# Performance work log

Hardware: AMD Instinct MI355X
Metric: run time of the kernel (lower is better)

The kernel has to match this reference:

```python
import jax, jax.numpy as jnp
import numpy as np

NUM_HEADS = 16
D_MODEL = 1024
D_K = D_MODEL // NUM_HEADS
THETA = 10000.0
SEQ_LEN = 2048
BATCH = 2


def _rope(x, token_positions):
    # x: [B, H, S, d_k]; token_positions: [S] int
    d_k = x.shape[-1]
    inv_freq = THETA ** (-jnp.arange(0, d_k, 2, dtype=jnp.float32) / d_k)  # [d_k/2]
    ang = token_positions.astype(jnp.float32)[:, None] * inv_freq[None, :]  # [S, d_k/2]
    cos, sin = jnp.cos(ang), jnp.sin(ang)
    x_even = x[..., ::2]
    x_odd = x[..., 1::2]
    rot_even = x_even * cos - x_odd * sin
    rot_odd = x_even * sin + x_odd * cos
    return jnp.stack([rot_even, rot_odd], axis=-1).reshape(x.shape)


def setup_inputs() -> dict:
    key = jax.random.key(0)
    kx, kq, kk, kv, ko = jax.random.split(key, 5)
    sigma = float(np.sqrt(2.0 / (D_MODEL + D_MODEL)))
    x = jax.random.normal(kx, (BATCH, SEQ_LEN, D_MODEL), dtype=jnp.float32)
    Wq = jax.random.truncated_normal(kq, -3.0, 3.0, (D_MODEL, D_MODEL), jnp.float32) * sigma
    Wk = jax.random.truncated_normal(kk, -3.0, 3.0, (D_MODEL, D_MODEL), jnp.float32) * sigma
    Wv = jax.random.truncated_normal(kv, -3.0, 3.0, (D_MODEL, D_MODEL), jnp.float32) * sigma
    Wo = jax.random.truncated_normal(ko, -3.0, 3.0, (D_MODEL, D_MODEL), jnp.float32) * sigma
    token_positions = jnp.arange(SEQ_LEN, dtype=jnp.int32)
    return {"x": x, "Wq": Wq, "Wk": Wk, "Wv": Wv, "Wo": Wo, "token_positions": token_positions}


def reference(x, Wq, Wk, Wv, Wo, token_positions):
    bs, seq_len, _ = x.shape
    # Linear stores W as [out, in]: out = einsum('...i,oi->...o')
    def proj(W):
        h = jnp.einsum('bsi,oi->bso', x, W)
        return h.reshape(bs, seq_len, NUM_HEADS, D_K).transpose(0, 2, 1, 3)  # [B,H,S,d_k]
    Q = _rope(proj(Wq), token_positions)
    K = _rope(proj(Wk), token_positions)
    V = proj(Wv)
    scores = jnp.einsum('bhqd,bhkd->bhqk', Q, K) / jnp.sqrt(jnp.float32(D_K))
    causal = jnp.tril(jnp.ones((seq_len, seq_len), dtype=bool))
    scores = jnp.where(causal[None, None], scores, -jnp.inf)
    probs = jax.nn.softmax(scores, axis=-1)
    attn = jnp.einsum('bhqk,bhkd->bhqd', probs, V)
    attn = attn.transpose(0, 2, 1, 3).reshape(bs, seq_len, NUM_HEADS * D_K)
    return jnp.einsum('bsi,oi->bso', attn, Wo)
```

## Files before the change

kernel.cpp:

```cpp
#include <hip/hip_runtime.h>
#include <math.h>

#define SEQ  2048
#define DM   1024
#define NH   16
#define DK   64
#define MTOT 4096
#define BATCH 2

typedef __attribute__((ext_vector_type(8))) short bf16x8;
typedef __attribute__((ext_vector_type(4))) float f32x4;

#define CSC 0.18033688011112042f
#define FMAX 12.0f

__device__ __forceinline__ ushort f2bf(float f) {
    unsigned u = __builtin_bit_cast(unsigned, f);
    u += 0x7FFFu + ((u >> 16) & 1u);
    return (ushort)(u >> 16);
}

__device__ __forceinline__ void async_ld16(const void* g, void* l) {
    __builtin_amdgcn_global_load_lds(
        (const __attribute__((address_space(1))) void*)g,
        (__attribute__((address_space(3))) void*)l, 16, 0, 0);
}


__global__ __launch_bounds__(256) void convert_kernel(
    const float* __restrict__ X, const float* __restrict__ Wq,
    const float* __restrict__ Wk, const float* __restrict__ Wv,
    const float* __restrict__ Wo, const int* __restrict__ pos,
    ushort* __restrict__ Xb, ushort* __restrict__ Wqkvb,
    ushort* __restrict__ Wob, float2* __restrict__ rtab)
{
    const int y = blockIdx.y;
    if (y == 5) {
        int i = blockIdx.x * 256 + threadIdx.x;
        if (i < SEQ * 32) {
            int s = i >> 5, j = i & 31;
            float freq = exp2f(-(float)(2 * j) * (13.287712379549449f / 64.0f));
            float ang = (float)pos[s] * freq;
            float sn, cs;
            sincosf(ang, &sn, &cs);
            rtab[i] = make_float2(cs, sn);
        }
        return;
    }
    const float* src; ushort* dst; int n;
    if (y == 0)      { src = X;  dst = Xb;                 n = MTOT * DM; }
    else if (y == 1) { src = Wq; dst = Wqkvb;              n = DM * DM; }
    else if (y == 2) { src = Wk; dst = Wqkvb + DM * DM;    n = DM * DM; }
    else if (y == 3) { src = Wv; dst = Wqkvb + 2 * DM * DM; n = DM * DM; }
    else             { src = Wo; dst = Wob;                n = DM * DM; }
    for (int i = (blockIdx.x * 256 + threadIdx.x) * 4; i < n; i += gridDim.x * 256 * 4) {
        float4 v = *(const float4*)(src + i);
        ushort4 o = { f2bf(v.x), f2bf(v.y), f2bf(v.z), f2bf(v.w) };
        *(ushort4*)(dst + i) = o;
    }
}

template <int MODE>
__global__ __launch_bounds__(256, 3) void gemm_mfma(
    const ushort* __restrict__ Agl, const ushort* __restrict__ Bgl,
    const float2* __restrict__ rtab, ushort* __restrict__ O0,
    ushort* __restrict__ O1, ushort* __restrict__ O2,
    float* __restrict__ Fout)
{
    constexpr int BM = (MODE == 0) ? 128 : 64;
    constexpr int BN = 128;
    constexpr int BK = 64;
    constexpr int WM = (MODE == 0) ? 64 : 32;
    constexpr int MT = WM / 16;
    constexpr int ROWS = BM + BN;
    constexpr int NINST = ROWS / 8;
    constexpr int PW = NINST / 4;

    __shared__ __align__(16) ushort S[ROWS * BK];

    const int t    = threadIdx.x;
    const int lane = t & 63;
    const int w    = t >> 6;
    const int wm   = w >> 1, wn = w & 1;
    const int l16  = lane & 15, quad = lane >> 4;
    const int lrow8  = lane >> 3;
    const int lchunk = lane & 7;

    const int bn = blockIdx.x, bm = blockIdx.y;
    const int m0 = bm * BM, n0 = bn * BN;

    f32x4 acc[MT][4];
#pragma unroll
    for (int mt = 0; mt < MT; ++mt)
#pragma unroll
        for (int nt = 0; nt < 4; ++nt) acc[mt][nt] = (f32x4){0.f, 0.f, 0.f, 0.f};

    for (int kt = 0; kt < DM / BK; ++kt) {
        __syncthreads();
#pragma unroll
        for (int i = 0; i < PW; ++i) {
            const int rbase = (w * PW + i) * 8;
            const int row = rbase + lrow8;
            const int sc = lchunk ^ (row & 7);
            const ushort* g;
            if (rbase < BM)
                g = Agl + (size_t)(m0 + row) * DM + kt * BK + sc * 8;
            else
                g = Bgl + (size_t)(n0 + row - BM) * DM + kt * BK + sc * 8;
            async_ld16(g, &S[rbase * BK]);
        }
        __syncthreads();

#pragma unroll
        for (int ks = 0; ks < 2; ++ks) {
            bf16x8 af[MT], bfr[4];
#pragma unroll
            for (int mt = 0; mt < MT; ++mt) {
                const int r = wm * WM + mt * 16 + l16;
                af[mt] = *(const bf16x8*)&S[r * BK + (((ks * 4 + quad) ^ (r & 7)) << 3)];
            }
#pragma unroll
            for (int nt = 0; nt < 4; ++nt) {
                const int r = BM + wn * 64 + nt * 16 + l16;
                bfr[nt] = *(const bf16x8*)&S[r * BK + (((ks * 4 + quad) ^ (r & 7)) << 3)];
            }
#pragma unroll
            for (int mt = 0; mt < MT; ++mt)
#pragma unroll
                for (int nt = 0; nt < 4; ++nt)
                    acc[mt][nt] = __builtin_amdgcn_mfma_f32_16x16x32_bf16(
                        af[mt], bfr[nt], acc[mt][nt], 0, 0, 0);
        }
    }

    if (MODE == 1) {
#pragma unroll
        for (int mt = 0; mt < MT; ++mt)
#pragma unroll
            for (int r = 0; r < 4; ++r) {
                const int m = m0 + wm * WM + mt * 16 + quad * 4 + r;
#pragma unroll
                for (int nt = 0; nt < 4; ++nt) {
                    const int n = n0 + wn * 64 + nt * 16 + l16;
                    Fout[(size_t)m * DM + n] = acc[mt][nt][r];
                }
            }
    } else {
        const int matb = n0 >> 10;
        if (matb < 2) {
            ushort* img = matb ? O1 : O0;
            const int hh = ((n0 & 1023) + wn * 64) >> 6;
            int dloc[4];
#pragma unroll
            for (int nt = 0; nt < 4; ++nt) dloc[nt] = nt * 16 + l16;
#pragma unroll
            for (int mt = 0; mt < MT; ++mt)
#pragma unroll
                for (int r = 0; r < 4; ++r) {
                    const int m = m0 + wm * WM + mt * 16 + quad * 4 + r;
                    const int bb = m >> 11;
                    const int s = m & 2047;
                    const size_t base =
                        ((size_t)(bb * NH + hh) * 32 + (s >> 6)) * 4096 + (s & 63) * 64;
                    const int swz = s & 7;
#pragma unroll
                    for (int nt = 0; nt < 4; ++nt) {
                        const float v = acc[mt][nt][r];
                        const float vp = __shfl_xor(v, 1);
                        const float2 cs = rtab[s * 32 + (dloc[nt] >> 1)];
                        float res = (dloc[nt] & 1) ? (vp * cs.y + v * cs.x)
                                                   : (v * cs.x - vp * cs.y);
                        if (matb == 0) res *= CSC;
                        const int d = dloc[nt];
                        img[base + (((d >> 3) ^ swz) << 3) + (d & 7)] = f2bf(res);
                    }
                }
        } else {
#pragma unroll
            for (int mt = 0; mt < MT; ++mt)
#pragma unroll
                for (int r = 0; r < 4; ++r) {
                    const int m = m0 + wm * WM + mt * 16 + quad * 4 + r;
                    const int bb = m >> 11;
                    const int s = m & 2047;
#pragma unroll
                    for (int nt = 0; nt < 4; ++nt) {
                        const int dgl = (n0 & 1023) + wn * 64 + nt * 16 + l16;
                        const int hh = dgl >> 6, dd = dgl & 63;
                        const size_t off =
                            ((size_t)(bb * NH + hh) * 32 + (s >> 6)) * 4096 + dd * 64 +
                            ((((s & 63) >> 3) ^ (dd & 7)) << 3) + (s & 7);
                        O2[off] = f2bf(acc[mt][nt][r]);
                    }
                }
        }
    }
}

__global__ __launch_bounds__(256, 2) void attn_mfma(
    const ushort* __restrict__ Qimg, const ushort* __restrict__ Kimg,
    const ushort* __restrict__ Vimg, ushort* __restrict__ Ob)
{
    const int t    = threadIdx.x;
    const int lane = t & 63;
    const int w    = t >> 6;
    const int l16  = lane & 15;
    const int quad = lane >> 4;
    const int swz  = l16 & 7;

    const int id = blockIdx.x;
    const int h  = id & 15;
    const int z  = id >> 4;
    const int b  = z & 1;
    const int p  = z >> 1;
    const int qtB = 31 - p;

    const size_t bh = ((size_t)(b * NH + h)) * 32;
    const ushort* Kh = Kimg + bh * 4096;
    const ushort* Vh = Vimg + bh * 4096;

    __shared__ __align__(16) ushort Ks[2][4096];
    __shared__ __align__(16) ushort Vs[2][4096];
    __shared__ __align__(16) ushort Ps[4096];

#define STAGE_KV(tile, buf)                                                  \
    do {                                                                     \
        const ushort* Kt_ = Kh + (size_t)(tile) * 4096;                      \
        const ushort* Vt_ = Vh + (size_t)(tile) * 4096;                      \
        _Pragma("unroll") for (int i_ = 0; i_ < 2; ++i_) {                   \
            async_ld16(Kt_ + i_ * 2048 + w * 512 + lane * 8,                 \
                       &Ks[buf][i_ * 2048 + w * 512]);                       \
            async_ld16(Vt_ + i_ * 2048 + w * 512 + lane * 8,                 \
                       &Vs[buf][i_ * 2048 + w * 512]);                       \
        }                                                                    \
    } while (0)

    const int qr = w * 16 + l16;

    bf16x8 bQ0, bQ1;
    {
        const ushort* Qt = Qimg + (bh + p) * 4096;
        bQ0 = *(const bf16x8*)(Qt + qr * 64 + ((quad ^ swz) << 3));
        bQ1 = *(const bf16x8*)(Qt + qr * 64 + (((4 + quad) ^ swz) << 3));
    }

    STAGE_KV(0, 0);

    f32x4 Oacc[4];
    float l_i = 0.f;
#pragma unroll
    for (int d = 0; d < 4; ++d) Oacc[d] = (f32x4){0.f, 0.f, 0.f, 0.f};

    int qt = p;

    auto writeO = [&](int qtw) {
        float lf = l_i;
        lf += __shfl_xor(lf, 16);
        lf += __shfl_xor(lf, 32);
#pragma unroll
        for (int r = 0; r < 4; ++r) {
            const float lr = __shfl(lf, (lane & 48) | (quad * 4 + r));
            const float inv = 1.0f / lr;
            const int q_abs = qtw * 64 + w * 16 + quad * 4 + r;
            ushort* dst = Ob + (size_t)(b * SEQ + q_abs) * DM + h * DK + l16;
#pragma unroll
            for (int dblk = 0; dblk < 4; ++dblk)
                dst[dblk * 16] = f2bf(Oacc[dblk][r] * inv);
        }
    };

    for (int it = 0; it <= 32; ++it) {
        const int cur = it & 1;
        const int kt = (it <= p) ? it : it - (p + 1);
        __syncthreads();

        if (it < 32) {
            const int itn = it + 1;
            const int ktn = (itn <= p) ? itn : itn - (p + 1);
            STAGE_KV(ktn, cur ^ 1);
        }

        bf16x8 aK[4][2];
#pragma unroll
        for (int ki = 0; ki < 4; ++ki)
#pragma unroll
            for (int ds = 0; ds < 2; ++ds)
                aK[ki][ds] = *(const bf16x8*)
                    &Ks[cur][(ki * 16 + l16) * 64 + (((ds * 4 + quad) ^ swz) << 3)];
        bf16x8 bV[2][4];
#pragma unroll
        for (int s2 = 0; s2 < 2; ++s2)
#pragma unroll
            for (int dblk = 0; dblk < 4; ++dblk)
                bV[s2][dblk] = *(const bf16x8*)
                    &Vs[cur][(dblk * 16 + l16) * 64 + (((s2 * 4 + quad) ^ swz) << 3)];

        f32x4 Sc[4];
#pragma unroll
        for (int ki = 0; ki < 4; ++ki) {
            Sc[ki] = (f32x4){0.f, 0.f, 0.f, 0.f};
            Sc[ki] = __builtin_amdgcn_mfma_f32_16x16x32_bf16(aK[ki][0], bQ0, Sc[ki], 0, 0, 0);
            Sc[ki] = __builtin_amdgcn_mfma_f32_16x16x32_bf16(aK[ki][1], bQ1, Sc[ki], 0, 0, 0);
        }

        const bool diag = (kt == qt);
        const int qa = w * 16 + l16;
        const int ka = quad * 4;
        const int prow = qr * 64;
        const int phalf = (quad & 1) * 4;
#pragma unroll
        for (int ki = 0; ki < 4; ++ki) {
            float pe[4];
#pragma unroll
            for (int r = 0; r < 4; ++r) {
                const bool masked = diag && (ka + ki * 16 + r > qa);
                pe[r] = masked ? 0.f
                               : __builtin_amdgcn_exp2f(Sc[ki][r] - FMAX);
                l_i += pe[r];
            }
            uint2 pk;
            pk.x = __builtin_amdgcn_perm(__builtin_bit_cast(unsigned, pe[1]),
                                         __builtin_bit_cast(unsigned, pe[0]),
                                         0x07060302u);
            pk.y = __builtin_amdgcn_perm(__builtin_bit_cast(unsigned, pe[3]),
                                         __builtin_bit_cast(unsigned, pe[2]),
                                         0x07060302u);
            const int seg = ki * 2 + (quad >> 1);
            *(uint2*)&Ps[prow + (((seg ^ swz) << 3) + phalf)] = pk;
        }

#pragma unroll
        for (int s2 = 0; s2 < 2; ++s2) {
            bf16x8 aP = *(const bf16x8*)&Ps[prow + (((s2 * 4 + quad) ^ swz) << 3)];
#pragma unroll
            for (int dblk = 0; dblk < 4; ++dblk)
                Oacc[dblk] = __builtin_amdgcn_mfma_f32_16x16x32_bf16(
                    aP, bV[s2][dblk], Oacc[dblk], 0, 0, 0);
        }

        if (it == p) {
            writeO(p);
            l_i = 0.f;
#pragma unroll
            for (int d = 0; d < 4; ++d) Oacc[d] = (f32x4){0.f, 0.f, 0.f, 0.f};
            qt = qtB;
            const ushort* Qt = Qimg + (bh + qtB) * 4096;
            bQ0 = *(const bf16x8*)(Qt + qr * 64 + ((quad ^ swz) << 3));
            bQ1 = *(const bf16x8*)(Qt + qr * 64 + (((4 + quad) ^ swz) << 3));
        }
    }

    writeO(qtB);
#undef STAGE_KV
}

extern "C" void kernel_launch(void* const* d_in, const int* in_sizes, int n_in,
                              void* d_out, int out_size, void* d_ws, size_t ws_size,
                              hipStream_t stream)
{
    const float* x  = (const float*)d_in[0];
    const float* Wq = (const float*)d_in[1];
    const float* Wk = (const float*)d_in[2];
    const float* Wv = (const float*)d_in[3];
    const float* Wo = (const float*)d_in[4];
    const int* pos  = (const int*)d_in[5];
    float* out = (float*)d_out;

    ushort* Xb    = (ushort*)d_ws;
    ushort* Wqkvb = Xb + (size_t)MTOT * DM;
    ushort* Wob   = Wqkvb + (size_t)3 * DM * DM;
    float2* rtab  = (float2*)(Wob + (size_t)DM * DM);
    ushort* Qimg  = (ushort*)(rtab + SEQ * 32);
    ushort* Kimg  = Qimg + (size_t)MTOT * DM;
    ushort* Vimg  = Kimg + (size_t)MTOT * DM;
    ushort* attnb = Vimg + (size_t)MTOT * DM;

    convert_kernel<<<dim3(1024, 6), dim3(256), 0, stream>>>(
        x, Wq, Wk, Wv, Wo, pos, Xb, Wqkvb, Wob, rtab);
    gemm_mfma<0><<<dim3(24, 32), dim3(256), 0, stream>>>(
        Xb, Wqkvb, rtab, Qimg, Kimg, Vimg, nullptr);
    attn_mfma<<<dim3(512), dim3(256), 0, stream>>>(Qimg, Kimg, Vimg, attnb);
    gemm_mfma<1><<<dim3(8, 64), dim3(256), 0, stream>>>(
        attnb, Wob, nullptr, nullptr, nullptr, nullptr, out);
}
```

Measured before the change: 169.9 us.

## Stage two KV tiles per barrier to halve attention loop synchronizations

The attention loop now processes K/V tiles in pairs. Two tiles are staged into a doubled LDS buffer per stage, so one __syncthreads covers two tile computations instead of one. This halves the barrier count and gives the async loads more compute to hide behind. In exchange LDS use roughly doubles (about 72KB), which may reduce occupancy. It also relies on the Ps scratch being reused across sub-iterations without a barrier, which works only because each wave reads and writes its own rows.

After: 167.5 us. No clear change (-1.4%).

```diff
diff --git a/kernel.cpp b/kernel.cpp
--- a/kernel.cpp
+++ b/kernel.cpp
@@ -219,19 +219,21 @@
     const ushort* Kh = Kimg + bh * 4096;
     const ushort* Vh = Vimg + bh * 4096;
 
-    __shared__ __align__(16) ushort Ks[2][4096];
-    __shared__ __align__(16) ushort Vs[2][4096];
+    __shared__ __align__(16) ushort Ks[2][2][4096];
+    __shared__ __align__(16) ushort Vs[2][2][4096];
     __shared__ __align__(16) ushort Ps[4096];
 
-#define STAGE_KV(tile, buf)                                                  \
+#define TILE_OF(it_) (((it_) <= p) ? (it_) : (it_) - (p + 1))
+
+#define STAGE_KV(tile, buf, sub)                                             \
     do {                                                                     \
         const ushort* Kt_ = Kh + (size_t)(tile) * 4096;                      \
         const ushort* Vt_ = Vh + (size_t)(tile) * 4096;                      \
         _Pragma("unroll") for (int i_ = 0; i_ < 2; ++i_) {                   \
             async_ld16(Kt_ + i_ * 2048 + w * 512 + lane * 8,                 \
-                       &Ks[buf][i_ * 2048 + w * 512]);                       \
+                       &Ks[buf][sub][i_ * 2048 + w * 512]);                  \
             async_ld16(Vt_ + i_ * 2048 + w * 512 + lane * 8,                 \
-                       &Vs[buf][i_ * 2048 + w * 512]);                       \
+                       &Vs[buf][sub][i_ * 2048 + w * 512]);                  \
         }                                                                    \
     } while (0)
 
@@ -244,7 +246,8 @@
         bQ1 = *(const bf16x8*)(Qt + qr * 64 + (((4 + quad) ^ swz) << 3));
     }
 
-    STAGE_KV(0, 0);
+    STAGE_KV(TILE_OF(0), 0, 0);
+    STAGE_KV(TILE_OF(1), 0, 1);
 
     f32x4 Oacc[4];
     float l_i = 0.f;
@@ -269,89 +272,96 @@
         }
     };
 
-    for (int it = 0; it <= 32; ++it) {
-        const int cur = it & 1;
-        const int kt = (it <= p) ? it : it - (p + 1);
+    for (int j = 0; j <= 16; ++j) {
+        const int buf = j & 1;
         __syncthreads();
 
-        if (it < 32) {
-            const int itn = it + 1;
-            const int ktn = (itn <= p) ? itn : itn - (p + 1);
-            STAGE_KV(ktn, cur ^ 1);
-        }
-
-        bf16x8 aK[4][2];
-#pragma unroll
-        for (int ki = 0; ki < 4; ++ki)
-#pragma unroll
-            for (int ds = 0; ds < 2; ++ds)
-                aK[ki][ds] = *(const bf16x8*)
-                    &Ks[cur][(ki * 16 + l16) * 64 + (((ds * 4 + quad) ^ swz) << 3)];
-        bf16x8 bV[2][4];
-#pragma unroll
-        for (int s2 = 0; s2 < 2; ++s2)
-#pragma unroll
-            for (int dblk = 0; dblk < 4; ++dblk)
-                bV[s2][dblk] = *(const bf16x8*)
-                    &Vs[cur][(dblk * 16 + l16) * 64 + (((s2 * 4 + quad) ^ swz) << 3)];
-
-        f32x4 Sc[4];
-#pragma unroll
-        for (int ki = 0; ki < 4; ++ki) {
-            Sc[ki] = (f32x4){0.f, 0.f, 0.f, 0.f};
-            Sc[ki] = __builtin_amdgcn_mfma_f32_16x16x32_bf16(aK[ki][0], bQ0, Sc[ki], 0, 0, 0);
-            Sc[ki] = __builtin_amdgcn_mfma_f32_16x16x32_bf16(aK[ki][1], bQ1, Sc[ki], 0, 0, 0);
-        }
-
-        const bool diag = (kt == qt);
-        const int qa = w * 16 + l16;
-        const int ka = quad * 4;
-        const int prow = qr * 64;
-        const int phalf = (quad & 1) * 4;
-#pragma unroll
-        for (int ki = 0; ki < 4; ++ki) {
-            float pe[4];
-#pragma unroll
-            for (int r = 0; r < 4; ++r) {
-                const bool masked = diag && (ka + ki * 16 + r > qa);
-                pe[r] = masked ? 0.f
-                               : __builtin_amdgcn_exp2f(Sc[ki][r] - FMAX);
-                l_i += pe[r];
-            }
-            uint2 pk;
-            pk.x = __builtin_amdgcn_perm(__builtin_bit_cast(unsigned, pe[1]),
-                                         __builtin_bit_cast(unsigned, pe[0]),
-                                         0x07060302u);
-            pk.y = __builtin_amdgcn_perm(__builtin_bit_cast(unsigned, pe[3]),
-                                         __builtin_bit_cast(unsigned, pe[2]),
-                                         0x07060302u);
-            const int seg = ki * 2 + (quad >> 1);
-            *(uint2*)&Ps[prow + (((seg ^ swz) << 3) + phalf)] = pk;
-        }
-
-#pragma unroll
-        for (int s2 = 0; s2 < 2; ++s2) {
-            bf16x8 aP = *(const bf16x8*)&Ps[prow + (((s2 * 4 + quad) ^ swz) << 3)];
-#pragma unroll
-            for (int dblk = 0; dblk < 4; ++dblk)
-                Oacc[dblk] = __builtin_amdgcn_mfma_f32_16x16x32_bf16(
-                    aP, bV[s2][dblk], Oacc[dblk], 0, 0, 0);
-        }
-
-        if (it == p) {
-            writeO(p);
-            l_i = 0.f;
-#pragma unroll
-            for (int d = 0; d < 4; ++d) Oacc[d] = (f32x4){0.f, 0.f, 0.f, 0.f};
-            qt = qtB;
-            const ushort* Qt = Qimg + (bh + qtB) * 4096;
-            bQ0 = *(const bf16x8*)(Qt + qr * 64 + ((quad ^ swz) << 3));
-            bQ1 = *(const bf16x8*)(Qt + qr * 64 + (((4 + quad) ^ swz) << 3));
+        if (j < 16) {
+            const int it0 = 2 * (j + 1);
+            STAGE_KV(TILE_OF(it0), buf ^ 1, 0);
+            if (it0 + 1 <= 32) STAGE_KV(TILE_OF(it0 + 1), buf ^ 1, 1);
+        }
+
+#pragma unroll
+        for (int sub = 0; sub < 2; ++sub) {
+            const int it = 2 * j + sub;
+            if (it > 32) break;
+            const int kt = TILE_OF(it);
+
+            bf16x8 aK[4][2];
+#pragma unroll
+            for (int ki = 0; ki < 4; ++ki)
+#pragma unroll
+                for (int ds = 0; ds < 2; ++ds)
+                    aK[ki][ds] = *(const bf16x8*)
+                        &Ks[buf][sub][(ki * 16 + l16) * 64 + (((ds * 4 + quad) ^ swz) << 3)];
+            bf16x8 bV[2][4];
+#pragma unroll
+            for (int s2 = 0; s2 < 2; ++s2)
+#pragma unroll
+                for (int dblk = 0; dblk < 4; ++dblk)
+                    bV[s2][dblk] = *(const bf16x8*)
+                        &Vs[buf][sub][(dblk * 16 + l16) * 64 + (((s2 * 4 + quad) ^ swz) << 3)];
+
+            f32x4 Sc[4];
+#pragma unroll
+            for (int ki = 0; ki < 4; ++ki) {
+                Sc[ki] = (f32x4){0.f, 0.f, 0.f, 0.f};
+                Sc[ki] = __builtin_amdgcn_mfma_f32_16x16x32_bf16(aK[ki][0], bQ0, Sc[ki], 0, 0, 0);
+                Sc[ki] = __builtin_amdgcn_mfma_f32_16x16x32_bf16(aK[ki][1], bQ1, Sc[ki], 0, 0, 0);
+            }
+
+            const bool diag = (kt == qt);
+            const int qa = w * 16 + l16;
+            const int ka = quad * 4;
+            const int prow = qr * 64;
+            const int phalf = (quad & 1) * 4;
+#pragma unroll
+            for (int ki = 0; ki < 4; ++ki) {
+                float pe[4];
+#pragma unroll
+                for (int r = 0; r < 4; ++r) {
+                    const bool masked = diag && (ka + ki * 16 + r > qa);
+                    pe[r] = masked ? 0.f
+                                   : __builtin_amdgcn_exp2f(Sc[ki][r] - FMAX);
+                    l_i += pe[r];
+                }
+                uint2 pk;
+                pk.x = __builtin_amdgcn_perm(__builtin_bit_cast(unsigned, pe[1]),
+                                             __builtin_bit_cast(unsigned, pe[0]),
+                                             0x07060302u);
+                pk.y = __builtin_amdgcn_perm(__builtin_bit_cast(unsigned, pe[3]),
+                                             __builtin_bit_cast(unsigned, pe[2]),
+                                             0x07060302u);
+                const int seg = ki * 2 + (quad >> 1);
+                *(uint2*)&Ps[prow + (((seg ^ swz) << 3) + phalf)] = pk;
+            }
+
+#pragma unroll
+            for (int s2 = 0; s2 < 2; ++s2) {
+                bf16x8 aP = *(const bf16x8*)&Ps[prow + (((s2 * 4 + quad) ^ swz) << 3)];
+#pragma unroll
+                for (int dblk = 0; dblk < 4; ++dblk)
+                    Oacc[dblk] = __builtin_amdgcn_mfma_f32_16x16x32_bf16(
+                        aP, bV[s2][dblk], Oacc[dblk], 0, 0, 0);
+            }
+
+            if (it == p) {
+                writeO(p);
+                l_i = 0.f;
+#pragma unroll
+                for (int d = 0; d < 4; ++d) Oacc[d] = (f32x4){0.f, 0.f, 0.f, 0.f};
+                qt = qtB;
+                const ushort* Qt = Qimg + (bh + qtB) * 4096;
+                bQ0 = *(const bf16x8*)(Qt + qr * 64 + ((quad ^ swz) << 3));
+                bQ1 = *(const bf16x8*)(Qt + qr * 64 + (((4 + quad) ^ swz) << 3));
+            }
         }
     }
 
     writeO(qtB);
 #undef STAGE_KV
+#undef TILE_OF
 }
 
 extern "C" void kernel_launch(void* const* d_in, const int* in_sizes, int n_in,
```
